# Kernel optimization log

Hardware: AMD Instinct MI355X
Metric: run time of the kernel (lower is better)

The kernel has to match this reference:

```python
import jax, jax.numpy as jnp
import numpy as np

E = 500_000
N = 30_000
R = 6
H = 256
OE = 256
OUT = 1
L = 3          # num_layers
A = 2          # num_aux + 1 branches


def setup_inputs() -> dict:
    key = jax.random.key(0)
    ks = jax.random.split(key, 9)
    x = jax.random.normal(ks[0], (E, H), dtype=jnp.float32)
    rbf = jax.random.normal(ks[1], (E, R), dtype=jnp.float32)
    i = jax.random.randint(ks[2], (E,), 0, N, dtype=jnp.int64)
    # parameters (stored in [in, out] convention)
    s = 1.0 / np.sqrt(H)
    W_rbf = jax.random.normal(ks[3], (R, H), dtype=jnp.float32) / np.sqrt(R)
    W_up = jax.random.normal(ks[4], (A, H, OE), dtype=jnp.float32) * s
    W_hidden = jax.random.normal(ks[5], (A, L, OE, OE), dtype=jnp.float32) / np.sqrt(OE)
    b_hidden = jnp.zeros((A, L, OE), dtype=jnp.float32)
    W_out = jax.random.normal(ks[6], (A, OE, OUT), dtype=jnp.float32) / np.sqrt(OE)
    return {"x": x, "rbf": rbf, "i": i, "num_nodes": N,
            "W_rbf": W_rbf, "W_up": W_up, "W_hidden": W_hidden,
            "b_hidden": b_hidden, "W_out": W_out}


def reference(x, rbf, i, num_nodes, W_rbf, W_up, W_hidden, b_hidden, W_out):
    # elementwise multiply of per-edge features by radial basis projection,
    # then segment-sum over edge target index -> per-node features [N, H]
    msg = (rbf @ W_rbf) * x                     # [E, H]
    h = jax.ops.segment_sum(msg, i, num_segments=num_nodes)  # [N, H]
    outs = []
    for a in range(A):
        y = h @ W_up[a]                          # [N, OE]
        for l in range(L):
            y = jax.nn.silu(y @ W_hidden[a, l] + b_hidden[a, l])
        outs.append(y @ W_out[a])               # [N, OUT]
    return tuple(outs)
```

## Files before the change

kernel.cpp:

```cpp
#include <hip/hip_runtime.h>

#define E_EDGES 500000
#define N_NODES 30000
#define H_DIM   256

typedef float  floatx4 __attribute__((ext_vector_type(4)));
typedef short  shortx4 __attribute__((ext_vector_type(4)));
typedef short  shortx8 __attribute__((ext_vector_type(8)));
typedef __bf16 bf16x8  __attribute__((ext_vector_type(8)));

__device__ inline short f2bf(float f) {
    unsigned u = __builtin_bit_cast(unsigned, f);
    u += 0x7fffu + ((u >> 16) & 1u);
    return (short)(u >> 16);
}
__device__ inline float bf2f(short s) {
    unsigned u = ((unsigned)(unsigned short)s) << 16;
    return __builtin_bit_cast(float, u);
}

__global__ __launch_bounds__(256) void prep_weights(
    const float* __restrict__ wup, const float* __restrict__ whid,
    short* __restrict__ wfrag)
{
    int g   = blockIdx.x * 256 + threadIdx.x;
    int mat = g >> 13;
    int grp = g & 8191;
    int a = mat >> 2, lay = mat & 3;
    const float* src = (lay == 0) ? (wup + a * 65536)
                                  : (whid + (a * 3 + lay - 1) * 65536);
    int ks  = grp >> 10;
    int rem = grp & 1023;
    int ntg = rem >> 6;
    int lane = rem & 63;
    int q = lane >> 4, c = lane & 15;
    int col = ntg * 16 + c;
    int k0  = ks * 32 + q * 8;
    shortx8 v;
#pragma unroll
    for (int j = 0; j < 8; j++) v[j] = f2bf(src[(k0 + j) * 256 + col]);
    ((shortx8*)wfrag)[g] = v;
}

__global__ __launch_bounds__(256) void hist_kernel(
    const int* __restrict__ idx, int* __restrict__ counts)
{
    int e = blockIdx.x * 256 + threadIdx.x;
    if (e < E_EDGES) atomicAdd(&counts[idx[e]], 1);
}

__global__ __launch_bounds__(1024) void scan_kernel(
    const int* __restrict__ counts, int* __restrict__ offsets,
    int* __restrict__ cursor)
{
    const int t = threadIdx.x;
    const int lane = t & 63, wave = t >> 6;
    const int base = t * 30;
    int local[30];
    int s = 0;
#pragma unroll
    for (int j = 0; j < 30; j++) {
        int c = (base + j < N_NODES) ? counts[base + j] : 0;
        local[j] = s;
        s += c;
    }
    int incl = s;
#pragma unroll
    for (int d = 1; d < 64; d <<= 1) {
        int v = __shfl_up(incl, d);
        if (lane >= d) incl += v;
    }
    __shared__ int part[16];
    if (lane == 63) part[wave] = incl;
    __syncthreads();
    if (t == 0) {
        int run = 0;
#pragma unroll
        for (int k = 0; k < 16; k++) { int v = part[k]; part[k] = run; run += v; }
    }
    __syncthreads();
    int excl = part[wave] + incl - s;
#pragma unroll
    for (int j = 0; j < 30; j++) {
        int n = base + j;
        if (n < N_NODES) { offsets[n] = excl + local[j]; cursor[n] = excl + local[j]; }
    }
    if (t == 1023) offsets[N_NODES] = excl + s;
}

__global__ __launch_bounds__(256) void scatter_ids(
    const int* __restrict__ idx, int* __restrict__ cursor,
    int* __restrict__ edge_list)
{
    int e = blockIdx.x * 256 + threadIdx.x;
    if (e >= E_EDGES) return;
    int pos = atomicAdd(&cursor[idx[e]], 1);
    edge_list[pos] = e;
}

__global__ __launch_bounds__(256) void gather_nodes(
    const float* __restrict__ x, const float* __restrict__ rbf,
    const int* __restrict__ edge_list, const int* __restrict__ offsets,
    const float* __restrict__ wrbf, float* __restrict__ h)
{
    int node = blockIdx.x * 4 + (threadIdx.x >> 6);
    if (node >= N_NODES) return;
    int lane = threadIdx.x & 63;

    const floatx4* wr4 = (const floatx4*)wrbf;
    floatx4 wr[6];
#pragma unroll
    for (int k = 0; k < 6; k++) wr[k] = wr4[k * 64 + lane];

    int beg = offsets[node], end = offsets[node + 1];
    floatx4 acc = {0.f, 0.f, 0.f, 0.f};
    for (int j = beg; j < end; j++) {
        int e = edge_list[j];
        float r0 = rbf[e * 6 + 0], r1 = rbf[e * 6 + 1], r2 = rbf[e * 6 + 2];
        float r3 = rbf[e * 6 + 3], r4 = rbf[e * 6 + 4], r5 = rbf[e * 6 + 5];
        floatx4 xv = ((const floatx4*)x)[(size_t)e * 64 + lane];
        floatx4 p = r0 * wr[0] + r1 * wr[1] + r2 * wr[2]
                  + r3 * wr[3] + r4 * wr[4] + r5 * wr[5];
        acc += p * xv;
    }
    ((floatx4*)h)[(size_t)node * 64 + lane] = acc;
}

__global__ __launch_bounds__(256, 2) void mlp_kernel(
    const float* __restrict__ h, const short* __restrict__ wfrag,
    const float* __restrict__ bias, const float* __restrict__ wout,
    float* __restrict__ out)
{
    __shared__ __align__(16) short ylds[2][64 * 264];
    const int t = threadIdx.x;
    const int wave = t >> 6, lane = t & 63, q = lane >> 4, c15 = lane & 15;
    const int n0 = blockIdx.x * 64;
    const floatx4 fzero = {0.f, 0.f, 0.f, 0.f};

    for (int a = 0; a < 2; a++) {
#pragma unroll
        for (int j = 0; j < 16; j++) {
            int f = t + j * 256;
            int r = f >> 6, c4 = f & 63;
            floatx4 v = fzero;
            if (n0 + r < N_NODES) v = ((const floatx4*)h)[(size_t)(n0 + r) * 64 + c4];
            shortx4 s4 = { f2bf(v.x), f2bf(v.y), f2bf(v.z), f2bf(v.w) };
            *(shortx4*)&ylds[0][r * 264 + c4 * 4] = s4;
        }
        __syncthreads();

        int src = 0;
        for (int lay = 0; lay < 4; lay++) {
            const bf16x8* wf = (const bf16x8*)(wfrag + (size_t)(a * 4 + lay) * 65536);
            floatx4 acc[4][4];
#pragma unroll
            for (int mt = 0; mt < 4; mt++)
#pragma unroll
                for (int nt = 0; nt < 4; nt++) acc[mt][nt] = fzero;

#pragma unroll
            for (int ks = 0; ks < 8; ks++) {
                bf16x8 afr[4], bfr[4];
#pragma unroll
                for (int mt = 0; mt < 4; mt++)
                    afr[mt] = *(const bf16x8*)&ylds[src][(mt * 16 + c15) * 264 + ks * 32 + q * 8];
#pragma unroll
                for (int nt = 0; nt < 4; nt++)
                    bfr[nt] = wf[(ks * 16 + wave * 4 + nt) * 64 + lane];
#pragma unroll
                for (int mt = 0; mt < 4; mt++)
#pragma unroll
                    for (int nt = 0; nt < 4; nt++)
                        acc[mt][nt] = __builtin_amdgcn_mfma_f32_16x16x32_bf16(
                            afr[mt], bfr[nt], acc[mt][nt], 0, 0, 0);
            }

            int dst = 1 - src;
            float bv[4];
#pragma unroll
            for (int nt = 0; nt < 4; nt++)
                bv[nt] = (lay >= 1) ? bias[(a * 3 + lay - 1) * 256 + wave * 64 + nt * 16 + c15]
                                    : 0.0f;
#pragma unroll
            for (int mt = 0; mt < 4; mt++) {
#pragma unroll
                for (int nt = 0; nt < 4; nt++) {
#pragma unroll
                    for (int rg = 0; rg < 4; rg++) {
                        float v = acc[mt][nt][rg] + bv[nt];
                        if (lay >= 1) v = v / (1.0f + __expf(-v));
                        int row = mt * 16 + q * 4 + rg;
                        int col = wave * 64 + nt * 16 + c15;
                        ylds[dst][row * 264 + col] = f2bf(v);
                    }
                }
            }
            __syncthreads();
            src = dst;
        }

        {
            int r  = wave * 16 + (lane >> 2);
            int cq = lane & 3;
            float s = 0.0f;
#pragma unroll 16
            for (int c = cq * 64; c < cq * 64 + 64; c++)
                s += bf2f(ylds[src][r * 264 + c]) * wout[a * 256 + c];
            s += __shfl_xor(s, 1);
            s += __shfl_xor(s, 2);
            if (cq == 0 && n0 + r < N_NODES) out[a * N_NODES + n0 + r] = s;
        }
        __syncthreads();
    }
}

extern "C" void kernel_launch(void* const* d_in, const int* in_sizes, int n_in,
                              void* d_out, int out_size, void* d_ws, size_t ws_size,
                              hipStream_t stream)
{
    const float* x    = (const float*)d_in[0];
    const float* rbf  = (const float*)d_in[1];
    const int*   idx  = (const int*)d_in[2];
    const float* wrbf = (const float*)d_in[4];
    const float* wup  = (const float*)d_in[5];
    const float* whid = (const float*)d_in[6];
    const float* bias = (const float*)d_in[7];
    const float* wout = (const float*)d_in[8];
    float* out = (float*)d_out;

    char* ws = (char*)d_ws;
    float* h         = (float*)ws;                                   ws += (size_t)N_NODES * H_DIM * sizeof(float);
    short* wfrag     = (short*)ws;                                   ws += (size_t)8 * 65536 * sizeof(short);
    int*   counts    = (int*)ws;                                     ws += (size_t)N_NODES * sizeof(int);
    int*   offsets   = (int*)ws;                                     ws += (size_t)(N_NODES + 1) * sizeof(int);
    int*   cursor    = (int*)ws;                                     ws += (size_t)N_NODES * sizeof(int);
    int*   edge_list = (int*)ws;

    hipMemsetAsync(counts, 0, (size_t)N_NODES * sizeof(int), stream);
    prep_weights<<<256, 256, 0, stream>>>(wup, whid, wfrag);
    hist_kernel<<<(E_EDGES + 255) / 256, 256, 0, stream>>>(idx, counts);
    scan_kernel<<<1, 1024, 0, stream>>>(counts, offsets, cursor);
    scatter_ids<<<(E_EDGES + 255) / 256, 256, 0, stream>>>(idx, cursor, edge_list);
    gather_nodes<<<(N_NODES + 3) / 4, 256, 0, stream>>>(x, rbf, edge_list, offsets, wrbf, h);
    mlp_kernel<<<(N_NODES + 63) / 64, 256, 0, stream>>>(h, wfrag, bias, wout, out);
}
```

Measured before the change: 876.4 us.

## Fuse all stages into one persistent kernel with grid barriers

Replaces the six separate launches (weight prep, histogram, scan, scatter, gather, MLP) with one persistent kernel of 1024 blocks that separates the stages with atomic-counter grid barriers. The scan becomes a two-level parallel scan across blocks, the aggregated node features are stored as bf16 to halve their traffic, x is read with nontemporal loads, and the MLP uses a single LDS buffer with an extra barrier and interleaves the two branches across tiles. This removes launch gaps and the single-block scan. In exchange it relies on all 1024 blocks being co-resident for the spin barriers and adds barrier overhead.

```diff
diff --git a/kernel.cpp b/kernel.cpp
--- a/kernel.cpp
+++ b/kernel.cpp
@@ -2,7 +2,8 @@
 
 #define E_EDGES 500000
 #define N_NODES 30000
-#define H_DIM   256
+#define GRID    1024
+#define NTHREAD 262144
 
 typedef float  floatx4 __attribute__((ext_vector_type(4)));
 typedef short  shortx4 __attribute__((ext_vector_type(4)));
@@ -19,193 +20,215 @@
     return __builtin_bit_cast(float, u);
 }
 
-__global__ __launch_bounds__(256) void prep_weights(
+__device__ inline void gbar(int* ctr, int nblk) {
+    __syncthreads();
+    if (threadIdx.x == 0) {
+        __threadfence();
+        atomicAdd(ctr, 1);
+        int it = 0;
+        while (__hip_atomic_load(ctr, __ATOMIC_RELAXED, __HIP_MEMORY_SCOPE_AGENT) < nblk) {
+            __builtin_amdgcn_s_sleep(2);
+            if (++it > (1 << 22)) break;
+        }
+        __threadfence();
+    }
+    __syncthreads();
+}
+
+__global__ __launch_bounds__(256, 4) void mega(
+    const float* __restrict__ x, const float* __restrict__ rbf,
+    const int* __restrict__ idx, const float* __restrict__ wrbf,
     const float* __restrict__ wup, const float* __restrict__ whid,
-    short* __restrict__ wfrag)
-{
-    int g   = blockIdx.x * 256 + threadIdx.x;
-    int mat = g >> 13;
-    int grp = g & 8191;
-    int a = mat >> 2, lay = mat & 3;
-    const float* src = (lay == 0) ? (wup + a * 65536)
-                                  : (whid + (a * 3 + lay - 1) * 65536);
-    int ks  = grp >> 10;
-    int rem = grp & 1023;
-    int ntg = rem >> 6;
-    int lane = rem & 63;
-    int q = lane >> 4, c = lane & 15;
-    int col = ntg * 16 + c;
-    int k0  = ks * 32 + q * 8;
-    shortx8 v;
-#pragma unroll
-    for (int j = 0; j < 8; j++) v[j] = f2bf(src[(k0 + j) * 256 + col]);
-    ((shortx8*)wfrag)[g] = v;
-}
-
-__global__ __launch_bounds__(256) void hist_kernel(
-    const int* __restrict__ idx, int* __restrict__ counts)
-{
-    int e = blockIdx.x * 256 + threadIdx.x;
-    if (e < E_EDGES) atomicAdd(&counts[idx[e]], 1);
-}
-
-__global__ __launch_bounds__(1024) void scan_kernel(
-    const int* __restrict__ counts, int* __restrict__ offsets,
+    const float* __restrict__ bias, const float* __restrict__ wout,
+    float* __restrict__ out,
+    short* __restrict__ h16, short* __restrict__ wfrag,
+    int* __restrict__ edge_list, int* __restrict__ counts,
+    int* __restrict__ ctrs, int* __restrict__ blocksum,
+    int* __restrict__ blockbase, int* __restrict__ offsets,
     int* __restrict__ cursor)
 {
-    const int t = threadIdx.x;
+    __shared__ __align__(16) short ylds[64 * 264];
+    __shared__ int wpart[4];
+
+    const int b    = blockIdx.x;
+    const int t    = threadIdx.x;
+    const int gtid = b * 256 + t;
     const int lane = t & 63, wave = t >> 6;
-    const int base = t * 30;
-    int local[30];
-    int s = 0;
-#pragma unroll
-    for (int j = 0; j < 30; j++) {
-        int c = (base + j < N_NODES) ? counts[base + j] : 0;
-        local[j] = s;
-        s += c;
-    }
-    int incl = s;
-#pragma unroll
-    for (int d = 1; d < 64; d <<= 1) {
-        int v = __shfl_up(incl, d);
-        if (lane >= d) incl += v;
-    }
-    __shared__ int part[16];
-    if (lane == 63) part[wave] = incl;
-    __syncthreads();
-    if (t == 0) {
-        int run = 0;
-#pragma unroll
-        for (int k = 0; k < 16; k++) { int v = part[k]; part[k] = run; run += v; }
-    }
-    __syncthreads();
-    int excl = part[wave] + incl - s;
-#pragma unroll
-    for (int j = 0; j < 30; j++) {
-        int n = base + j;
-        if (n < N_NODES) { offsets[n] = excl + local[j]; cursor[n] = excl + local[j]; }
-    }
-    if (t == 1023) offsets[N_NODES] = excl + s;
-}
-
-__global__ __launch_bounds__(256) void scatter_ids(
-    const int* __restrict__ idx, int* __restrict__ cursor,
-    int* __restrict__ edge_list)
-{
-    int e = blockIdx.x * 256 + threadIdx.x;
-    if (e >= E_EDGES) return;
-    int pos = atomicAdd(&cursor[idx[e]], 1);
-    edge_list[pos] = e;
-}
-
-__global__ __launch_bounds__(256) void gather_nodes(
-    const float* __restrict__ x, const float* __restrict__ rbf,
-    const int* __restrict__ edge_list, const int* __restrict__ offsets,
-    const float* __restrict__ wrbf, float* __restrict__ h)
-{
-    int node = blockIdx.x * 4 + (threadIdx.x >> 6);
-    if (node >= N_NODES) return;
-    int lane = threadIdx.x & 63;
-
-    const floatx4* wr4 = (const floatx4*)wrbf;
-    floatx4 wr[6];
-#pragma unroll
-    for (int k = 0; k < 6; k++) wr[k] = wr4[k * 64 + lane];
-
-    int beg = offsets[node], end = offsets[node + 1];
-    floatx4 acc = {0.f, 0.f, 0.f, 0.f};
-    for (int j = beg; j < end; j++) {
-        int e = edge_list[j];
-        float r0 = rbf[e * 6 + 0], r1 = rbf[e * 6 + 1], r2 = rbf[e * 6 + 2];
-        float r3 = rbf[e * 6 + 3], r4 = rbf[e * 6 + 4], r5 = rbf[e * 6 + 5];
-        floatx4 xv = ((const floatx4*)x)[(size_t)e * 64 + lane];
-        floatx4 p = r0 * wr[0] + r1 * wr[1] + r2 * wr[2]
-                  + r3 * wr[3] + r4 * wr[4] + r5 * wr[5];
-        acc += p * xv;
-    }
-    ((floatx4*)h)[(size_t)node * 64 + lane] = acc;
-}
-
-__global__ __launch_bounds__(256, 2) void mlp_kernel(
-    const float* __restrict__ h, const short* __restrict__ wfrag,
-    const float* __restrict__ bias, const float* __restrict__ wout,
-    float* __restrict__ out)
-{
-    __shared__ __align__(16) short ylds[2][64 * 264];
-    const int t = threadIdx.x;
-    const int wave = t >> 6, lane = t & 63, q = lane >> 4, c15 = lane & 15;
-    const int n0 = blockIdx.x * 64;
-    const floatx4 fzero = {0.f, 0.f, 0.f, 0.f};
-
-    for (int a = 0; a < 2; a++) {
-#pragma unroll
-        for (int j = 0; j < 16; j++) {
-            int f = t + j * 256;
-            int r = f >> 6, c4 = f & 63;
-            floatx4 v = fzero;
-            if (n0 + r < N_NODES) v = ((const floatx4*)h)[(size_t)(n0 + r) * 64 + c4];
-            shortx4 s4 = { f2bf(v.x), f2bf(v.y), f2bf(v.z), f2bf(v.w) };
-            *(shortx4*)&ylds[0][r * 264 + c4 * 4] = s4;
-        }
+
+    if (gtid < 65536) {
+        int mat = gtid >> 13, grp = gtid & 8191;
+        int a = mat >> 2, lay = mat & 3;
+        const float* src = (lay == 0) ? (wup + a * 65536)
+                                      : (whid + (a * 3 + lay - 1) * 65536);
+        int ks  = grp >> 10;
+        int rem = grp & 1023;
+        int ntg = rem >> 6;
+        int l2  = rem & 63;
+        int q2 = l2 >> 4, c2 = l2 & 15;
+        int col = ntg * 16 + c2;
+        int k0  = ks * 32 + q2 * 8;
+        shortx8 v;
+#pragma unroll
+        for (int j = 0; j < 8; j++) v[j] = f2bf(src[(k0 + j) * 256 + col]);
+        ((shortx8*)wfrag)[gtid] = v;
+    }
+
+    for (int e = gtid; e < E_EDGES; e += NTHREAD)
+        atomicAdd(&counts[idx[e]], 1);
+    gbar(ctrs + 0, GRID);
+
+    if (b < 1000) {
+        if (wave == 0) {
+            int n = b * 30 + lane;
+            int c = (lane < 30) ? counts[n] : 0;
+            int incl = c;
+#pragma unroll
+            for (int d = 1; d < 64; d <<= 1) {
+                int v = __shfl_up(incl, d);
+                if (lane >= d) incl += v;
+            }
+            if (lane < 30) offsets[n] = incl - c;
+            if (lane == 29) blocksum[b] = incl;
+        }
+    } else if (t == 0) {
+        blocksum[b] = 0;
+    }
+    gbar(ctrs + 1, GRID);
+
+    if (b == 0) {
+        int4 v = ((const int4*)blocksum)[t];
+        int s1 = v.x + v.y, s2 = s1 + v.z, tot = s2 + v.w;
+        int incl = tot;
+#pragma unroll
+        for (int d = 1; d < 64; d <<= 1) {
+            int u = __shfl_up(incl, d);
+            if (lane >= d) incl += u;
+        }
+        if (lane == 63) wpart[wave] = incl;
         __syncthreads();
-
-        int src = 0;
+        int base = 0;
+#pragma unroll
+        for (int k = 0; k < 4; k++) if (k < wave) base += wpart[k];
+        int excl = base + incl - tot;
+        int4 o;
+        o.x = excl; o.y = excl + v.x; o.z = excl + s1; o.w = excl + s2;
+        ((int4*)blockbase)[t] = o;
+    }
+    gbar(ctrs + 2, GRID);
+
+    if (b < 1000 && wave == 0 && lane < 30) {
+        int n = b * 30 + lane;
+        int o = offsets[n] + blockbase[b];
+        offsets[n] = o;
+        cursor[n]  = o;
+    }
+    if (gtid == 0) offsets[N_NODES] = E_EDGES;
+    gbar(ctrs + 3, GRID);
+
+    for (int e = gtid; e < E_EDGES; e += NTHREAD) {
+        int pos = atomicAdd(&cursor[idx[e]], 1);
+        edge_list[pos] = e;
+    }
+    gbar(ctrs + 4, GRID);
+
+    {
+        const floatx4* wr4 = (const floatx4*)wrbf;
+        floatx4 wr[6];
+#pragma unroll
+        for (int k = 0; k < 6; k++) wr[k] = wr4[k * 64 + lane];
+
+        for (int node = b * 4 + wave; node < N_NODES; node += 4096) {
+            int beg = offsets[node], end = offsets[node + 1];
+            floatx4 acc = {0.f, 0.f, 0.f, 0.f};
+            for (int j = beg; j < end; j++) {
+                int e = edge_list[j];
+                float r0 = rbf[e * 6 + 0], r1 = rbf[e * 6 + 1], r2 = rbf[e * 6 + 2];
+                float r3 = rbf[e * 6 + 3], r4 = rbf[e * 6 + 4], r5 = rbf[e * 6 + 5];
+                floatx4 xv = __builtin_nontemporal_load(
+                    &((const floatx4*)x)[(size_t)e * 64 + lane]);
+                floatx4 p = r0 * wr[0] + r1 * wr[1] + r2 * wr[2]
+                          + r3 * wr[3] + r4 * wr[4] + r5 * wr[5];
+                acc += p * xv;
+            }
+            shortx4 s4 = { f2bf(acc.x), f2bf(acc.y), f2bf(acc.z), f2bf(acc.w) };
+            ((shortx4*)h16)[(size_t)node * 64 + lane] = s4;
+        }
+    }
+    gbar(ctrs + 5, GRID);
+
+    const int q = lane >> 4, c15 = lane & 15;
+    for (int tile = b; tile < 938; tile += GRID) {
+        const int a  = tile & 1;
+        const int n0 = (tile >> 1) * 64;
+
+#pragma unroll
+        for (int j = 0; j < 8; j++) {
+            int grp = t + j * 256;
+            int r = grp >> 5, c8 = grp & 31;
+            shortx8 v = {0, 0, 0, 0, 0, 0, 0, 0};
+            if (n0 + r < N_NODES)
+                v = *(const shortx8*)&h16[(size_t)(n0 + r) * 256 + c8 * 8];
+            *(shortx8*)&ylds[r * 264 + c8 * 8] = v;
+        }
+        __syncthreads();
+
         for (int lay = 0; lay < 4; lay++) {
             const bf16x8* wf = (const bf16x8*)(wfrag + (size_t)(a * 4 + lay) * 65536);
             floatx4 acc[4][4];
 #pragma unroll
             for (int mt = 0; mt < 4; mt++)
 #pragma unroll
-                for (int nt = 0; nt < 4; nt++) acc[mt][nt] = fzero;
+                for (int nt = 0; nt < 4; nt++)
+                    acc[mt][nt] = (floatx4){0.f, 0.f, 0.f, 0.f};
 
 #pragma unroll
             for (int ks = 0; ks < 8; ks++) {
-                bf16x8 afr[4], bfr[4];
-#pragma unroll
-                for (int mt = 0; mt < 4; mt++)
-                    afr[mt] = *(const bf16x8*)&ylds[src][(mt * 16 + c15) * 264 + ks * 32 + q * 8];
+                bf16x8 bfr[4];
 #pragma unroll
                 for (int nt = 0; nt < 4; nt++)
                     bfr[nt] = wf[(ks * 16 + wave * 4 + nt) * 64 + lane];
 #pragma unroll
-                for (int mt = 0; mt < 4; mt++)
+                for (int mt = 0; mt < 4; mt++) {
+                    bf16x8 afr = *(const bf16x8*)&ylds[(mt * 16 + c15) * 264 + ks * 32 + q * 8];
 #pragma unroll
                     for (int nt = 0; nt < 4; nt++)
                         acc[mt][nt] = __builtin_amdgcn_mfma_f32_16x16x32_bf16(
-                            afr[mt], bfr[nt], acc[mt][nt], 0, 0, 0);
-            }
-
-            int dst = 1 - src;
+                            afr, bfr[nt], acc[mt][nt], 0, 0, 0);
+                }
+            }
+            __syncthreads();
+
             float bv[4];
 #pragma unroll
             for (int nt = 0; nt < 4; nt++)
-                bv[nt] = (lay >= 1) ? bias[(a * 3 + lay - 1) * 256 + wave * 64 + nt * 16 + c15]
-                                    : 0.0f;
-#pragma unroll
-            for (int mt = 0; mt < 4; mt++) {
-#pragma unroll
-                for (int nt = 0; nt < 4; nt++) {
+                bv[nt] = (lay >= 1)
+                       ? bias[(a * 3 + lay - 1) * 256 + wave * 64 + nt * 16 + c15]
+                       : 0.0f;
+#pragma unroll
+            for (int mt = 0; mt < 4; mt++)
+#pragma unroll
+                for (int nt = 0; nt < 4; nt++)
 #pragma unroll
                     for (int rg = 0; rg < 4; rg++) {
                         float v = acc[mt][nt][rg] + bv[nt];
                         if (lay >= 1) v = v / (1.0f + __expf(-v));
-                        int row = mt * 16 + q * 4 + rg;
-                        int col = wave * 64 + nt * 16 + c15;
-                        ylds[dst][row * 264 + col] = f2bf(v);
+                        ylds[(mt * 16 + q * 4 + rg) * 264 + wave * 64 + nt * 16 + c15] = f2bf(v);
                     }
-                }
-            }
             __syncthreads();
-            src = dst;
         }
 
         {
             int r  = wave * 16 + (lane >> 2);
             int cq = lane & 3;
+            const float* wo = wout + a * 256 + cq * 64;
+            const short* yp = &ylds[r * 264 + cq * 64];
             float s = 0.0f;
-#pragma unroll 16
-            for (int c = cq * 64; c < cq * 64 + 64; c++)
-                s += bf2f(ylds[src][r * 264 + c]) * wout[a * 256 + c];
+#pragma unroll
+            for (int bb = 0; bb < 8; bb++) {
+                shortx8 v = *(const shortx8*)&yp[bb * 8];
+#pragma unroll
+                for (int j = 0; j < 8; j++) s += bf2f(v[j]) * wo[bb * 8 + j];
+            }
             s += __shfl_xor(s, 1);
             s += __shfl_xor(s, 2);
             if (cq == 0 && n0 + r < N_NODES) out[a * N_NODES + n0 + r] = s;
@@ -218,6 +241,7 @@
                               void* d_out, int out_size, void* d_ws, size_t ws_size,
                               hipStream_t stream)
 {
+    (void)in_sizes; (void)n_in; (void)out_size; (void)ws_size;
     const float* x    = (const float*)d_in[0];
     const float* rbf  = (const float*)d_in[1];
     const int*   idx  = (const int*)d_in[2];
@@ -229,18 +253,18 @@
     float* out = (float*)d_out;
 
     char* ws = (char*)d_ws;
-    float* h         = (float*)ws;                                   ws += (size_t)N_NODES * H_DIM * sizeof(float);
-    short* wfrag     = (short*)ws;                                   ws += (size_t)8 * 65536 * sizeof(short);
-    int*   counts    = (int*)ws;                                     ws += (size_t)N_NODES * sizeof(int);
-    int*   offsets   = (int*)ws;                                     ws += (size_t)(N_NODES + 1) * sizeof(int);
-    int*   cursor    = (int*)ws;                                     ws += (size_t)N_NODES * sizeof(int);
-    int*   edge_list = (int*)ws;
-
-    hipMemsetAsync(counts, 0, (size_t)N_NODES * sizeof(int), stream);
-    prep_weights<<<256, 256, 0, stream>>>(wup, whid, wfrag);
-    hist_kernel<<<(E_EDGES + 255) / 256, 256, 0, stream>>>(idx, counts);
-    scan_kernel<<<1, 1024, 0, stream>>>(counts, offsets, cursor);
-    scatter_ids<<<(E_EDGES + 255) / 256, 256, 0, stream>>>(idx, cursor, edge_list);
-    gather_nodes<<<(N_NODES + 3) / 4, 256, 0, stream>>>(x, rbf, edge_list, offsets, wrbf, h);
-    mlp_kernel<<<(N_NODES + 63) / 64, 256, 0, stream>>>(h, wfrag, bias, wout, out);
-}
+    short* h16       = (short*)ws;  ws += (size_t)N_NODES * 256 * sizeof(short);
+    short* wfrag     = (short*)ws;  ws += (size_t)8 * 65536 * sizeof(short);
+    int*   edge_list = (int*)ws;    ws += (size_t)E_EDGES * sizeof(int);
+    int*   counts    = (int*)ws;    ws += (size_t)N_NODES * sizeof(int);
+    int*   ctrs      = (int*)ws;    ws += 8 * sizeof(int);
+    int*   blocksum  = (int*)ws;    ws += 1024 * sizeof(int);
+    int*   blockbase = (int*)ws;    ws += 1024 * sizeof(int);
+    int*   offsets   = (int*)ws;    ws += (size_t)(N_NODES + 1) * sizeof(int);
+    int*   cursor    = (int*)ws;
+
+    hipMemsetAsync(counts, 0, (size_t)(N_NODES + 8) * sizeof(int), stream);
+    mega<<<GRID, 256, 0, stream>>>(x, rbf, idx, wrbf, wup, whid, bias, wout, out,
+                                   h16, wfrag, edge_list, counts, ctrs,
+                                   blocksum, blockbase, offsets, cursor);
+}
```

New measurement: 1.444 ms. 1.65x slower.
